# Optimization experiments

Measured on AMD Instinct MI355X. Metric: run time of the kernel, lower is better.

The kernel has to match this reference:

```python
import jax, jax.numpy as jnp
import numpy as np
from jax import lax

B_, L_, C_IN = 32, 1024, 3
D_MODEL, D_STATE, D_CONV, EXPAND = 256, 16, 4, 2
D_INNER = EXPAND * D_MODEL           # 512
DT_RANK = D_MODEL // 16              # 16
N_HEADS, N_CLASS = 8, 10
LN_EPS = 1e-5


def _pos_emb(L, d):
    pos = np.arange(L, dtype=np.float32)[:, None]
    div = np.exp(np.arange(0, d, 2, dtype=np.float32) * (-np.log(10000.0) / d))
    pe = np.zeros((L, d), np.float32)
    pe[:, 0::2] = np.sin(pos * div)
    pe[:, 1::2] = np.cos(pos * div)
    return jnp.asarray(pe)


def setup_inputs() -> dict:
    key = jax.random.key(0)
    ks = jax.random.split(key, 12)
    f = lambda k, shp, s: jax.random.normal(k, shp, jnp.float32) * s
    return {
        'x_enc': f(ks[0], (B_, L_, C_IN), 1.0),
        'x_mark_enc': jnp.ones((B_, L_), jnp.float32),
        'conv_emb_w': f(ks[1], (D_MODEL, C_IN, 3), (2.0 / (C_IN * 3)) ** 0.5),
        'in_proj_w': f(ks[2], (2 * D_INNER, D_MODEL), D_MODEL ** -0.5),
        'conv1d_w': f(ks[3], (D_INNER, 1, D_CONV), D_CONV ** -0.5),
        'conv1d_b': f(ks[4], (D_INNER,), 0.02),
        'x_proj_w': f(ks[5], (DT_RANK + 2 * D_STATE, D_INNER), D_INNER ** -0.5),
        'dt_proj_w': f(ks[6], (D_INNER, DT_RANK), DT_RANK ** -0.5),
        'dt_proj_b': f(ks[7], (D_INNER,), 0.1) - 2.0,
        'A_log': jnp.log(jnp.tile(jnp.arange(1, D_STATE + 1, dtype=jnp.float32), (D_INNER, 1))),
        'D': jnp.ones((D_INNER,), jnp.float32),
        'out_proj_w': f(ks[8], (D_MODEL, D_INNER), D_INNER ** -0.5),
        'ln_g': jnp.ones((D_MODEL,), jnp.float32),
        'ln_b': jnp.zeros((D_MODEL,), jnp.float32),
        'out_w': f(ks[9], (N_CLASS, D_MODEL), D_MODEL ** -0.5),
        'attn_w': f(ks[10], (N_HEADS, D_MODEL), 0.02),
        'attn_b': jnp.ones((N_HEADS,), jnp.float32),
    }


def _forward(x_enc, x_mark_enc, conv_emb_w, in_proj_w, conv1d_w, conv1d_b,
             x_proj_w, dt_proj_w, dt_proj_b, A_log, D, out_proj_w,
             ln_g, ln_b, out_w, attn_w, attn_b):
    silu = jax.nn.silu
    # --- embedding: Conv1d 'same' with replicate padding + sinusoidal PE ---
    xp = jnp.pad(x_enc, ((0, 0), (1, 1), (0, 0)), mode='edge')      # k=3 -> pad (1,1)
    x = lax.conv_general_dilated(xp.transpose(0, 2, 1), conv_emb_w, (1,), 'VALID',
                                 dimension_numbers=('NCH', 'OIH', 'NCH')).transpose(0, 2, 1)
    x = x + _pos_emb(L_, D_MODEL)[None]                              # (B,L,D)

    # --- Mamba_TimeVariant (standard Mamba selective scan) ---
    xz = jnp.einsum('bld,ed->ble', x, in_proj_w)                     # (B,L,2*Din)
    xin, z = xz[..., :D_INNER], xz[..., D_INNER:]
    # depthwise causal conv, kernel D_CONV
    xc = jnp.pad(xin.transpose(0, 2, 1), ((0, 0), (0, 0), (D_CONV - 1, 0)))
    xc = lax.conv_general_dilated(xc, conv1d_w, (1,), 'VALID',
                                  feature_group_count=D_INNER,
                                  dimension_numbers=('NCH', 'OIH', 'NCH'))
    xc = silu(xc.transpose(0, 2, 1) + conv1d_b)                      # (B,L,Din)

    dbl = jnp.einsum('bld,ed->ble', xc, x_proj_w)                    # (B,L,dt_rank+2*N)
    dtr = dbl[..., :DT_RANK]
    Bm = dbl[..., DT_RANK:DT_RANK + D_STATE]                         # (B,L,N)
    Cm = dbl[..., DT_RANK + D_STATE:]                                # (B,L,N)
    dt = jax.nn.softplus(jnp.einsum('blr,dr->bld', dtr, dt_proj_w) + dt_proj_b)
    A = -jnp.exp(A_log)                                              # (Din,N)

    def step(h, inp):
        dt_t, B_t, C_t, x_t = inp                                    # (B,Din),(B,N),(B,N),(B,Din)
        dA = jnp.exp(dt_t[..., None] * A)                            # (B,Din,N)
        h = dA * h + dt_t[..., None] * B_t[:, None, :] * x_t[..., None]
        y = jnp.einsum('bdn,bn->bd', h, C_t)
        return h, y

    h0 = jnp.zeros((B_, D_INNER, D_STATE), xc.dtype)
    inputs = (dt.transpose(1, 0, 2), Bm.transpose(1, 0, 2),
              Cm.transpose(1, 0, 2), xc.transpose(1, 0, 2))
    _, ys = lax.scan(step, h0, inputs)                               # (L,B,Din)
    y = ys.transpose(1, 0, 2) + xc * D                               # skip via D
    y = y * silu(z)
    m = jnp.einsum('bld,ed->ble', y, out_proj_w)                     # (B,L,Dmodel)

    # LayerNorm + SiLU
    mu = m.mean(-1, keepdims=True)
    var = ((m - mu) ** 2).mean(-1, keepdims=True)
    m = (m - mu) * lax.rsqrt(var + LN_EPS) * ln_g + ln_b
    m = silu(m)

    # classification head
    logit = jnp.einsum('bld,cd->blc', m, out_w) * x_mark_enc[..., None]
    s = jnp.einsum('bld,hd->blh', m, attn_w) + attn_b                # (B,L,H)
    w = jax.nn.softmax(jnp.max(s, axis=2, keepdims=True), axis=1)    # (B,L,1)
    return (logit * w).sum(1)                                        # (B,num_class)


def reference(x_enc, x_mark_enc, conv_emb_w, in_proj_w, conv1d_w, conv1d_b,
              x_proj_w, dt_proj_w, dt_proj_b, A_log, D, out_proj_w,
              ln_g, ln_b, out_w, attn_w, attn_b):
    return _forward(x_enc, x_mark_enc, conv_emb_w, in_proj_w, conv1d_w, conv1d_b,
                    x_proj_w, dt_proj_w, dt_proj_b, A_log, D, out_proj_w,
                    ln_g, ln_b, out_w, attn_w, attn_b)
```

## Files before the change

### kernel.cpp

```cpp
#include <hip/hip_runtime.h>
#include <hip/hip_bf16.h>
#include <math.h>

#define B_  32
#define L_  1024
#define CIN 3
#define DM  256
#define DI  512
#define NST 16
#define NH  8
#define NC  10
#define M_TOT (B_*L_)

typedef unsigned short u16;
typedef __attribute__((ext_vector_type(8))) short bf16x8;
typedef __attribute__((ext_vector_type(4))) float f32x4;

static __device__ __forceinline__ float sigmoidf_(float x) {
    return 1.0f / (1.0f + __expf(-x));
}
static __device__ __forceinline__ u16 f2bf(float f) {
    unsigned int u = __float_as_uint(f);
    return (u16)((u + 0x7FFF + ((u >> 16) & 1)) >> 16);
}
static __device__ __forceinline__ float bf2f(u16 u) {
    return __uint_as_float(((unsigned int)u) << 16);
}

static __device__ __forceinline__ void reduce16_pair(float& a, float& b) {
    asm volatile(
        "s_nop 1\n\t"
        "v_add_f32 %0, %0, %0 quad_perm:[1,0,3,2] row_mask:0xf bank_mask:0xf\n\t"
        "v_add_f32 %1, %1, %1 quad_perm:[1,0,3,2] row_mask:0xf bank_mask:0xf\n\t"
        "s_nop 1\n\t"
        "v_add_f32 %0, %0, %0 quad_perm:[2,3,0,1] row_mask:0xf bank_mask:0xf\n\t"
        "v_add_f32 %1, %1, %1 quad_perm:[2,3,0,1] row_mask:0xf bank_mask:0xf\n\t"
        "s_nop 1\n\t"
        "v_add_f32 %0, %0, %0 row_ror:4 row_mask:0xf bank_mask:0xf\n\t"
        "v_add_f32 %1, %1, %1 row_ror:4 row_mask:0xf bank_mask:0xf\n\t"
        "s_nop 1\n\t"
        "v_add_f32 %0, %0, %0 row_ror:8 row_mask:0xf bank_mask:0xf\n\t"
        "v_add_f32 %1, %1, %1 row_ror:8 row_mask:0xf bank_mask:0xf\n\t"
        "s_nop 1\n\t"
        : "+v"(a), "+v"(b));
}

__global__ __launch_bounds__(256) void k_cvt(const float* __restrict__ in,
        u16* __restrict__ out) {
    int i = (blockIdx.x * 256 + threadIdx.x) * 4;
    float4 v = *(const float4*)(in + i);
    ushort4 o;
    o.x = f2bf(v.x); o.y = f2bf(v.y); o.z = f2bf(v.z); o.w = f2bf(v.w);
    *(ushort4*)(out + i) = o;
}

__global__ __launch_bounds__(256) void k_embed(const float* __restrict__ xe,
        const float* __restrict__ w, u16* __restrict__ x) {
    int bl = blockIdx.x;
    int l = bl & (L_-1);
    int b = bl >> 10;
    int d = threadIdx.x;
    const float* xb = xe + (size_t)b * L_ * CIN;
    int t0 = l > 0 ? l-1 : 0;
    int t2 = l < L_-1 ? l+1 : L_-1;
    const float* w3 = w + d*9;
    float acc = 0.f;
    #pragma unroll
    for (int i = 0; i < 3; ++i) {
        acc += xb[t0*3+i] * w3[i*3+0];
        acc += xb[l *3+i] * w3[i*3+1];
        acc += xb[t2*3+i] * w3[i*3+2];
    }
    int j = d >> 1;
    float div = expf((float)(2*j) * (-logf(10000.0f)/(float)DM));
    float ang = (float)l * div;
    acc += (d & 1) ? cosf(ang) : sinf(ang);
    x[(size_t)bl*DM + d] = f2bf(acc);
}

#define GST 40
__global__ __launch_bounds__(256) void k_gemm_mfma(
        const u16* __restrict__ A, const u16* __restrict__ W,
        float* __restrict__ O1f, u16* __restrict__ O1b,
        u16* __restrict__ O2b, int M, int N, int K, int S) {
    __shared__ u16 As[128*GST];
    __shared__ u16 Bs[128*GST];
    int tid = threadIdx.x;
    int row0 = blockIdx.y * 128, col0 = blockIdx.x * 128;
    int wave = tid >> 6, lane = tid & 63;
    int wr = (wave >> 1) * 64, wc = (wave & 1) * 64;
    int l16 = lane & 15, kl = lane >> 4;
    int srow = tid >> 1, skh = (tid & 1) * 16;
    const u16* Ag = A + (size_t)(row0 + srow) * K + skh;
    const u16* Wg = W + (size_t)(col0 + srow) * K + skh;

    f32x4 acc[4][4];
    #pragma unroll
    for (int m = 0; m < 4; ++m)
        #pragma unroll
        for (int n = 0; n < 4; ++n)
            acc[m][n] = (f32x4){0.f, 0.f, 0.f, 0.f};

    for (int k0 = 0; k0 < K; k0 += 32) {
        uint4 a0 = *(const uint4*)(Ag + k0);
        uint4 a1 = *(const uint4*)(Ag + k0 + 8);
        uint4 b0 = *(const uint4*)(Wg + k0);
        uint4 b1 = *(const uint4*)(Wg + k0 + 8);
        __syncthreads();
        *(uint4*)&As[srow*GST + skh]     = a0;
        *(uint4*)&As[srow*GST + skh + 8] = a1;
        *(uint4*)&Bs[srow*GST + skh]     = b0;
        *(uint4*)&Bs[srow*GST + skh + 8] = b1;
        __syncthreads();
        bf16x8 af[4], bf[4];
        #pragma unroll
        for (int m = 0; m < 4; ++m)
            af[m] = *(const bf16x8*)&As[(wr + m*16 + l16)*GST + kl*8];
        #pragma unroll
        for (int n = 0; n < 4; ++n)
            bf[n] = *(const bf16x8*)&Bs[(wc + n*16 + l16)*GST + kl*8];
        #pragma unroll
        for (int m = 0; m < 4; ++m)
            #pragma unroll
            for (int n = 0; n < 4; ++n)
                acc[m][n] = __builtin_amdgcn_mfma_f32_16x16x32_bf16(
                                af[m], bf[n], acc[m][n], 0, 0, 0);
    }

    #pragma unroll
    for (int m = 0; m < 4; ++m) {
        int rbase = row0 + wr + m*16 + kl*4;
        #pragma unroll
        for (int n = 0; n < 4; ++n) {
            int col = col0 + wc + n*16 + l16;
            #pragma unroll
            for (int r = 0; r < 4; ++r) {
                float v = acc[m][n][r];
                if (col < S) {
                    if (O1b) O1b[(size_t)(rbase + r)*S + col] = f2bf(v);
                    else     O1f[(size_t)(rbase + r)*S + col] = v;
                } else {
                    O2b[(size_t)(rbase + r)*(N - S) + (col - S)] = f2bf(v);
                }
            }
        }
    }
}

__global__ __launch_bounds__(256) void k_conv(const u16* __restrict__ xin,
        const float* __restrict__ w, const float* __restrict__ bias,
        u16* __restrict__ xc) {
    size_t i4 = (size_t)blockIdx.x * 256 + threadIdx.x;
    int d4 = (int)(i4 & (DI/4 - 1)) * 4;
    size_t m = i4 >> 7;
    int l = (int)(m & (L_-1));
    float4 wv0 = *(const float4*)(w + (size_t)(d4+0)*4);
    float4 wv1 = *(const float4*)(w + (size_t)(d4+1)*4);
    float4 wv2 = *(const float4*)(w + (size_t)(d4+2)*4);
    float4 wv3 = *(const float4*)(w + (size_t)(d4+3)*4);
    float W[4][4] = {{wv0.x,wv0.y,wv0.z,wv0.w},{wv1.x,wv1.y,wv1.z,wv1.w},
                     {wv2.x,wv2.y,wv2.z,wv2.w},{wv3.x,wv3.y,wv3.z,wv3.w}};
    float4 acc = *(const float4*)(bias + d4);
    #pragma unroll
    for (int k = 0; k < 4; ++k) {
        int t = l + k - 3;
        if (t >= 0) {
            ushort4 xv = *(const ushort4*)(xin + (m + k - 3)*DI + d4);
            acc.x = fmaf(bf2f(xv.x), W[0][k], acc.x);
            acc.y = fmaf(bf2f(xv.y), W[1][k], acc.y);
            acc.z = fmaf(bf2f(xv.z), W[2][k], acc.z);
            acc.w = fmaf(bf2f(xv.w), W[3][k], acc.w);
        }
    }
    ushort4 r;
    r.x = f2bf(acc.x * sigmoidf_(acc.x));
    r.y = f2bf(acc.y * sigmoidf_(acc.y));
    r.z = f2bf(acc.z * sigmoidf_(acc.z));
    r.w = f2bf(acc.w * sigmoidf_(acc.w));
    *(ushort4*)(xc + m*DI + d4) = r;
}

#define XBM 128
#define XBK 16
__global__ __launch_bounds__(256) void k_xproj(const u16* __restrict__ xc,
        const float* __restrict__ wp, float* __restrict__ dbl) {
    __shared__ float As[XBK][XBM];
    __shared__ float Ws[XBK][48];
    int tid = threadIdx.x;
    int row0 = blockIdx.x * XBM;
    int lr = tid >> 1;
    int lk = (tid & 1) * 8;
    int we = tid >> 2;
    int wk = (tid & 3) * 4;
    int tx = tid & 15;
    int ty = tid >> 4;
    float acc[8][3];
    #pragma unroll
    for (int i = 0; i < 8; ++i)
        #pragma unroll
        for (int j = 0; j < 3; ++j) acc[i][j] = 0.f;

    for (int k0 = 0; k0 < DI; k0 += XBK) {
        ushort4 ab0 = *(const ushort4*)(xc + (size_t)(row0+lr)*DI + k0 + lk);
        ushort4 ab1 = *(const ushort4*)(xc + (size_t)(row0+lr)*DI + k0 + lk + 4);
        float4 w0 = make_float4(0.f,0.f,0.f,0.f);
        if (tid < 192) w0 = *(const float4*)(wp + (size_t)we*DI + k0 + wk);
        __syncthreads();
        As[lk+0][lr]=bf2f(ab0.x); As[lk+1][lr]=bf2f(ab0.y);
        As[lk+2][lr]=bf2f(ab0.z); As[lk+3][lr]=bf2f(ab0.w);
        As[lk+4][lr]=bf2f(ab1.x); As[lk+5][lr]=bf2f(ab1.y);
        As[lk+6][lr]=bf2f(ab1.z); As[lk+7][lr]=bf2f(ab1.w);
        if (tid < 192) {
            Ws[wk+0][we]=w0.x; Ws[wk+1][we]=w0.y; Ws[wk+2][we]=w0.z; Ws[wk+3][we]=w0.w;
        }
        __syncthreads();
        #pragma unroll
        for (int k = 0; k < XBK; ++k) {
            float4 av0 = *(const float4*)&As[k][ty*8];
            float4 av1 = *(const float4*)&As[k][ty*8+4];
            float w0_ = Ws[k][tx*3+0];
            float w1_ = Ws[k][tx*3+1];
            float w2_ = Ws[k][tx*3+2];
            float ar[8] = {av0.x,av0.y,av0.z,av0.w,av1.x,av1.y,av1.z,av1.w};
            #pragma unroll
            for (int i = 0; i < 8; ++i) {
                acc[i][0] = fmaf(ar[i], w0_, acc[i][0]);
                acc[i][1] = fmaf(ar[i], w1_, acc[i][1]);
                acc[i][2] = fmaf(ar[i], w2_, acc[i][2]);
            }
        }
    }
    #pragma unroll
    for (int i = 0; i < 8; ++i) {
        size_t r = row0 + ty*8 + i;
        #pragma unroll
        for (int j = 0; j < 3; ++j)
            dbl[r*48 + tx*3 + j] = acc[i][j];
    }
}

__global__ __launch_bounds__(256) void k_dtproj(const float* __restrict__ dbl,
        const float* __restrict__ dtw, const float* __restrict__ dtb,
        float* __restrict__ dt) {
    __shared__ float wl[DI][17];
    __shared__ float rl[32][16];
    size_t m0 = (size_t)blockIdx.x * 32;
    for (int i = threadIdx.x; i < DI*16; i += 256)
        wl[i >> 4][i & 15] = dtw[i];
    for (int i = threadIdx.x; i < 32*16; i += 256)
        rl[i >> 4][i & 15] = dbl[(m0 + (i>>4))*48 + (i & 15)];
    __syncthreads();
    float b0 = dtb[threadIdx.x];
    float b1 = dtb[256 + threadIdx.x];
    for (int mm = 0; mm < 32; ++mm) {
        #pragma unroll
        for (int half = 0; half < 2; ++half) {
            int d = half*256 + threadIdx.x;
            float acc = half ? b1 : b0;
            #pragma unroll
            for (int r = 0; r < 16; ++r)
                acc = fmaf(rl[mm][r], wl[d][r], acc);
            float sp = fmaxf(acc, 0.f) + log1pf(__expf(-fabsf(acc)));
            dt[(m0+mm)*DI + d] = sp;
        }
    }
}

#define SCAN_T 64
__global__ __launch_bounds__(256) void k_scan(const float* __restrict__ dt,
        const u16* __restrict__ xcb, const float* __restrict__ dbl,
        const float* __restrict__ A_log, const float* __restrict__ Dp,
        const u16* __restrict__ zbf, u16* __restrict__ ybf) {
    __shared__ float4 sq4[SCAN_T*17];
    __shared__ float2 sBC2[SCAN_T*17];

    int tid = threadIdx.x;
    int ch = tid >> 4;
    int n  = tid & 15;
    int d0 = blockIdx.x * 16;
    int b  = blockIdx.y;
    int d  = d0 + ch;
    float Avl2 = -expf(A_log[(size_t)d*NST + n]) * 1.44269504f;
    float h = 0.f;
    size_t base = (size_t)b * L_;

    int st = tid >> 2;
    int sc = (tid & 3) * 4;
    float4 Dv = *(const float4*)(Dp + d0 + sc);

    for (int t0 = 0; t0 < L_; t0 += SCAN_T) {
        __syncthreads();
        {
            size_t row = base + t0 + st;
            float4 dtv = *(const float4*)(dt + row*DI + d0 + sc);
            ushort4 xv4 = *(const ushort4*)(xcb + row*DI + d0 + sc);
            ushort4 zv4 = *(const ushort4*)(zbf + row*DI + d0 + sc);
            float4 Bv  = *(const float4*)(dbl + row*48 + 16 + sc);
            float4 Cv  = *(const float4*)(dbl + row*48 + 32 + sc);
            float x0 = bf2f(xv4.x), x1 = bf2f(xv4.y);
            float x2 = bf2f(xv4.z), x3 = bf2f(xv4.w);
            float z0 = bf2f(zv4.x), z1 = bf2f(zv4.y);
            float z2 = bf2f(zv4.z), z3 = bf2f(zv4.w);
            float g0 = z0 * sigmoidf_(z0);
            float g1 = z1 * sigmoidf_(z1);
            float g2 = z2 * sigmoidf_(z2);
            float g3 = z3 * sigmoidf_(z3);
            sq4[st*17 + sc+0] = make_float4(dtv.x, dtv.x*x0, x0*Dv.x*g0, g0);
            sq4[st*17 + sc+1] = make_float4(dtv.y, dtv.y*x1, x1*Dv.y*g1, g1);
            sq4[st*17 + sc+2] = make_float4(dtv.z, dtv.z*x2, x2*Dv.z*g2, g2);
            sq4[st*17 + sc+3] = make_float4(dtv.w, dtv.w*x3, x3*Dv.w*g3, g3);
            sBC2[st*17 + sc+0] = make_float2(Bv.x, Cv.x);
            sBC2[st*17 + sc+1] = make_float2(Bv.y, Cv.y);
            sBC2[st*17 + sc+2] = make_float2(Bv.z, Cv.z);
            sBC2[st*17 + sc+3] = make_float2(Bv.w, Cv.w);
        }
        __syncthreads();

        #pragma unroll 2
        for (int t2 = 0; t2 < SCAN_T/2; ++t2) {
            float2 bc0 = sBC2[(2*t2)*17 + n];
            float2 bc1 = sBC2[(2*t2+1)*17 + n];
            float4 q0 = sq4[(2*t2)*17 + ch];
            float4 q1 = sq4[(2*t2+1)*17 + ch];
            float dA = exp2f(q0.x * Avl2);
            h = fmaf(dA, h, q0.y * bc0.x);
            float p0 = h * bc0.y;
            dA = exp2f(q1.x * Avl2);
            h = fmaf(dA, h, q1.y * bc1.x);
            float p1 = h * bc1.y;
            reduce16_pair(p0, p1);
            if (n == 0) {
                size_t row = base + t0 + 2*t2;
                ybf[row*DI + d]     = f2bf(fmaf(p0, q0.w, q0.z));
                ybf[(row+1)*DI + d] = f2bf(fmaf(p1, q1.w, q1.z));
            }
        }
    }
}

__global__ __launch_bounds__(256) void k_lnsilu(float* __restrict__ m,
        const float* __restrict__ g, const float* __restrict__ bta) {
    size_t row = (size_t)blockIdx.x*4 + (threadIdx.x >> 6);
    int lane = threadIdx.x & 63;
    float4 v = *(const float4*)(m + row*DM + lane*4);
    float s = v.x + v.y + v.z + v.w;
    #pragma unroll
    for (int o = 32; o > 0; o >>= 1) s += __shfl_xor(s, o);
    float mu = s * (1.0f/DM);
    float4 c = make_float4(v.x-mu, v.y-mu, v.z-mu, v.w-mu);
    float s2 = c.x*c.x + c.y*c.y + c.z*c.z + c.w*c.w;
    #pragma unroll
    for (int o = 32; o > 0; o >>= 1) s2 += __shfl_xor(s2, o);
    float rstd = 1.0f / sqrtf(s2 * (1.0f/DM) + 1e-5f);
    float4 gv = *(const float4*)(g + lane*4);
    float4 bv = *(const float4*)(bta + lane*4);
    float o0 = c.x*rstd*gv.x + bv.x;
    float o1 = c.y*rstd*gv.y + bv.y;
    float o2 = c.z*rstd*gv.z + bv.z;
    float o3 = c.w*rstd*gv.w + bv.w;
    float4 r;
    r.x = o0 * sigmoidf_(o0);
    r.y = o1 * sigmoidf_(o1);
    r.z = o2 * sigmoidf_(o2);
    r.w = o3 * sigmoidf_(o3);
    *(float4*)(m + row*DM + lane*4) = r;
}

#define HBK 32
__global__ __launch_bounds__(256) void k_heads18(const float* __restrict__ m,
        const float* __restrict__ aw, const float* __restrict__ ow,
        float* __restrict__ r18) {
    __shared__ float As[128][36];
    __shared__ float Ws[18][36];
    int tid = threadIdx.x;
    int row0 = blockIdx.x * 128;
    int r = tid >> 1, ch = tid & 1, cb = ch * 9;
    int sr = tid >> 1, sk = (tid & 1) * 16;
    float acc[9];
    #pragma unroll
    for (int c = 0; c < 9; ++c) acc[c] = 0.f;

    for (int k0 = 0; k0 < DM; k0 += HBK) {
        float4 a[4];
        #pragma unroll
        for (int q = 0; q < 4; ++q)
            a[q] = *(const float4*)(m + (size_t)(row0+sr)*DM + k0 + sk + q*4);
        float4 wv = make_float4(0.f,0.f,0.f,0.f);
        int wc = tid >> 3, wk = (tid & 7) * 4;
        if (tid < 144) {
            const float* wsrc = (wc < NH) ? (aw + wc*DM) : (ow + (wc-NH)*DM);
            wv = *(const float4*)(wsrc + k0 + wk);
        }
        __syncthreads();
        #pragma unroll
        for (int q = 0; q < 4; ++q)
            *(float4*)&As[sr][sk + q*4] = a[q];
        if (tid < 144)
            *(float4*)&Ws[wc][wk] = wv;
        __syncthreads();
        #pragma unroll
        for (int k4 = 0; k4 < HBK/4; ++k4) {
            float4 av = *(const float4*)&As[r][k4*4];
            #pragma unroll
            for (int c = 0; c < 9; ++c) {
                float4 w4 = *(const float4*)&Ws[cb + c][k4*4];
                acc[c] += av.x*w4.x + av.y*w4.y + av.z*w4.z + av.w*w4.w;
            }
        }
        __syncthreads();
    }
    #pragma unroll
    for (int c = 0; c < 9; ++c)
        r18[(size_t)(row0 + r)*18 + cb + c] = acc[c];
}

__global__ __launch_bounds__(256) void k_final(const float* __restrict__ r18,
        const float* __restrict__ ab, const float* __restrict__ xmark,
        float* __restrict__ out) {
    __shared__ float e[L_];
    __shared__ float red[256];
    int b = blockIdx.x;
    int tid = threadIdx.x;
    float abr[NH];
    #pragma unroll
    for (int j = 0; j < NH; ++j) abr[j] = ab[j];
    float mx = -1e30f;
    for (int l = tid; l < L_; l += 256) {
        const float* rr = r18 + ((size_t)b*L_ + l)*18;
        float sm = rr[0] + abr[0];
        #pragma unroll
        for (int j = 1; j < NH; ++j) sm = fmaxf(sm, rr[j] + abr[j]);
        e[l] = sm;
        mx = fmaxf(mx, sm);
    }
    #pragma unroll
    for (int o = 32; o > 0; o >>= 1) mx = fmaxf(mx, __shfl_xor(mx, o));
    red[tid] = mx;
    __syncthreads();
    mx = fmaxf(fmaxf(red[0], red[64]), fmaxf(red[128], red[192]));
    __syncthreads();
    float ssum = 0.f;
    for (int l = tid; l < L_; l += 256) {
        float ev = __expf(e[l] - mx);
        e[l] = ev;
        ssum += ev;
    }
    #pragma unroll
    for (int o = 32; o > 0; o >>= 1) ssum += __shfl_xor(ssum, o);
    if ((tid & 63) == 0) red[tid >> 6] = ssum;
    __syncthreads();
    float inv = 1.0f / (red[0]+red[1]+red[2]+red[3]);
    float acc[NC];
    #pragma unroll
    for (int c = 0; c < NC; ++c) acc[c] = 0.f;
    for (int l = tid; l < L_; l += 256) {
        float wl = e[l] * xmark[(size_t)b*L_ + l];
        const float* lg = r18 + ((size_t)b*L_ + l)*18 + NH;
        #pragma unroll
        for (int c = 0; c < NC; ++c) acc[c] = fmaf(wl, lg[c], acc[c]);
    }
    __syncthreads();
    for (int c = 0; c < NC; ++c) {
        red[tid] = acc[c];
        __syncthreads();
        if (tid < 64) {
            float s2 = red[tid]+red[tid+64]+red[tid+128]+red[tid+192];
            #pragma unroll
            for (int o = 32; o > 0; o >>= 1) s2 += __shfl_xor(s2, o);
            if (tid == 0) out[(size_t)b*NC + c] = s2 * inv;
        }
        __syncthreads();
    }
}

extern "C" void kernel_launch(void* const* d_in, const int* in_sizes, int n_in,
                              void* d_out, int out_size, void* d_ws, size_t ws_size,
                              hipStream_t stream) {
    const float* x_enc  = (const float*)d_in[0];
    const float* x_mark = (const float*)d_in[1];
    const float* cemb_w = (const float*)d_in[2];
    const float* inp_w  = (const float*)d_in[3];
    const float* c1_w   = (const float*)d_in[4];
    const float* c1_b   = (const float*)d_in[5];
    const float* xp_w   = (const float*)d_in[6];
    const float* dtp_w  = (const float*)d_in[7];
    const float* dtp_b  = (const float*)d_in[8];
    const float* A_log  = (const float*)d_in[9];
    const float* Dp     = (const float*)d_in[10];
    const float* outp_w = (const float*)d_in[11];
    const float* ln_g   = (const float*)d_in[12];
    const float* ln_b   = (const float*)d_in[13];
    const float* out_w  = (const float*)d_in[14];
    const float* attn_w = (const float*)d_in[15];
    const float* attn_b = (const float*)d_in[16];
    float* out = (float*)d_out;

    char* ws = (char*)d_ws;
    size_t o = 0;
    u16*   xbf  = (u16*)(ws + o);   o += (size_t)M_TOT*DM*2;
    u16*   xinb = (u16*)(ws + o);   o += (size_t)M_TOT*DI*2;
    u16*   zbf  = (u16*)(ws + o);   o += (size_t)M_TOT*DI*2;
    u16*   xcb  = (u16*)(ws + o);   o += (size_t)M_TOT*DI*2;
    u16*   ybf  = (u16*)(ws + o);   o += (size_t)M_TOT*DI*2;
    float* dt   = (float*)(ws + o); o += (size_t)M_TOT*DI*4;
    float* mm   = (float*)(ws + o); o += (size_t)M_TOT*DM*4;
    float* dbl  = (float*)(ws + o); o += (size_t)M_TOT*48*4;
    u16*   wbfi = (u16*)(ws + o);   o += (size_t)2*DI*DM*2;
    u16*   wbfo = (u16*)(ws + o);   o += (size_t)DM*DI*2;
    float* r18  = (float*)(ws + o); o += (size_t)M_TOT*18*4;

    k_cvt   <<<(2*DI*DM)/1024, 256, 0, stream>>>(inp_w, wbfi);
    k_cvt   <<<(DM*DI)/1024, 256, 0, stream>>>(outp_w, wbfo);
    k_embed <<<M_TOT, 256, 0, stream>>>(x_enc, cemb_w, xbf);
    k_gemm_mfma<<<dim3(8, M_TOT/128), 256, 0, stream>>>(xbf, wbfi,
                                nullptr, xinb, zbf, M_TOT, 2*DI, DM, DI);
    k_conv  <<<(M_TOT*DI/4)/256, 256, 0, stream>>>(xinb, c1_w, c1_b, xcb);
    k_xproj <<<M_TOT/XBM, 256, 0, stream>>>(xcb, xp_w, dbl);
    k_dtproj<<<M_TOT/32, 256, 0, stream>>>(dbl, dtp_w, dtp_b, dt);
    k_scan  <<<dim3(DI/16, B_), 256, 0, stream>>>(dt, xcb, dbl, A_log, Dp,
                                                  zbf, ybf);
    k_gemm_mfma<<<dim3(2, M_TOT/128), 256, 0, stream>>>(ybf, wbfo,
                                mm, nullptr, zbf, M_TOT, DM, DI, DM);
    k_lnsilu<<<M_TOT/4, 256, 0, stream>>>(mm, ln_g, ln_b);
    k_heads18<<<M_TOT/128, 256, 0, stream>>>(mm, attn_w, out_w, r18);
    k_final <<<B_, 256, 0, stream>>>(r18, attn_b, x_mark, out);
}
```

Before: 465.1 us.

## Give each scan thread two SSM states and 32 channels per block

Result: no change. 463.3 us (-0.4%).

```diff
diff --git a/kernel.cpp b/kernel.cpp
--- a/kernel.cpp
+++ b/kernel.cpp
@@ -27,7 +27,7 @@
     return __uint_as_float(((unsigned int)u) << 16);
 }
 
-static __device__ __forceinline__ void reduce16_pair(float& a, float& b) {
+static __device__ __forceinline__ void reduce8_pair(float& a, float& b) {
     asm volatile(
         "s_nop 1\n\t"
         "v_add_f32 %0, %0, %0 quad_perm:[1,0,3,2] row_mask:0xf bank_mask:0xf\n\t"
@@ -36,11 +36,8 @@
         "v_add_f32 %0, %0, %0 quad_perm:[2,3,0,1] row_mask:0xf bank_mask:0xf\n\t"
         "v_add_f32 %1, %1, %1 quad_perm:[2,3,0,1] row_mask:0xf bank_mask:0xf\n\t"
         "s_nop 1\n\t"
-        "v_add_f32 %0, %0, %0 row_ror:4 row_mask:0xf bank_mask:0xf\n\t"
-        "v_add_f32 %1, %1, %1 row_ror:4 row_mask:0xf bank_mask:0xf\n\t"
-        "s_nop 1\n\t"
-        "v_add_f32 %0, %0, %0 row_ror:8 row_mask:0xf bank_mask:0xf\n\t"
-        "v_add_f32 %1, %1, %1 row_ror:8 row_mask:0xf bank_mask:0xf\n\t"
+        "v_add_f32 %0, %0, %0 row_half_mirror row_mask:0xf bank_mask:0xf\n\t"
+        "v_add_f32 %1, %1, %1 row_half_mirror row_mask:0xf bank_mask:0xf\n\t"
         "s_nop 1\n\t"
         : "+v"(a), "+v"(b));
 }
@@ -271,65 +268,79 @@
         const u16* __restrict__ xcb, const float* __restrict__ dbl,
         const float* __restrict__ A_log, const float* __restrict__ Dp,
         const u16* __restrict__ zbf, u16* __restrict__ ybf) {
-    __shared__ float4 sq4[SCAN_T*17];
-    __shared__ float2 sBC2[SCAN_T*17];
+    __shared__ float4 sq4[SCAN_T*33];
+    __shared__ float2 sBC2[SCAN_T*18];
 
     int tid = threadIdx.x;
-    int ch = tid >> 4;
-    int n  = tid & 15;
-    int d0 = blockIdx.x * 16;
+    int wave = tid >> 6, lane = tid & 63;
+    int chw = lane >> 3;
+    int j   = lane & 7;
+    int ch  = wave*8 + chw;
+    int d0 = blockIdx.x * 32;
     int b  = blockIdx.y;
     int d  = d0 + ch;
-    float Avl2 = -expf(A_log[(size_t)d*NST + n]) * 1.44269504f;
-    float h = 0.f;
+    float Aa = -expf(A_log[(size_t)d*NST + 2*j])     * 1.44269504f;
+    float Ab = -expf(A_log[(size_t)d*NST + 2*j + 1]) * 1.44269504f;
+    float h0 = 0.f, h1 = 0.f;
     size_t base = (size_t)b * L_;
 
     int st = tid >> 2;
-    int sc = (tid & 3) * 4;
-    float4 Dv = *(const float4*)(Dp + d0 + sc);
+    int sc = (tid & 3) * 8;
+    int ns = (tid & 3) * 4;
+    float4 Dva = *(const float4*)(Dp + d0 + sc);
+    float4 Dvb = *(const float4*)(Dp + d0 + sc + 4);
 
     for (int t0 = 0; t0 < L_; t0 += SCAN_T) {
         __syncthreads();
         {
             size_t row = base + t0 + st;
-            float4 dtv = *(const float4*)(dt + row*DI + d0 + sc);
-            ushort4 xv4 = *(const ushort4*)(xcb + row*DI + d0 + sc);
-            ushort4 zv4 = *(const ushort4*)(zbf + row*DI + d0 + sc);
-            float4 Bv  = *(const float4*)(dbl + row*48 + 16 + sc);
-            float4 Cv  = *(const float4*)(dbl + row*48 + 32 + sc);
-            float x0 = bf2f(xv4.x), x1 = bf2f(xv4.y);
-            float x2 = bf2f(xv4.z), x3 = bf2f(xv4.w);
-            float z0 = bf2f(zv4.x), z1 = bf2f(zv4.y);
-            float z2 = bf2f(zv4.z), z3 = bf2f(zv4.w);
-            float g0 = z0 * sigmoidf_(z0);
-            float g1 = z1 * sigmoidf_(z1);
-            float g2 = z2 * sigmoidf_(z2);
-            float g3 = z3 * sigmoidf_(z3);
-            sq4[st*17 + sc+0] = make_float4(dtv.x, dtv.x*x0, x0*Dv.x*g0, g0);
-            sq4[st*17 + sc+1] = make_float4(dtv.y, dtv.y*x1, x1*Dv.y*g1, g1);
-            sq4[st*17 + sc+2] = make_float4(dtv.z, dtv.z*x2, x2*Dv.z*g2, g2);
-            sq4[st*17 + sc+3] = make_float4(dtv.w, dtv.w*x3, x3*Dv.w*g3, g3);
-            sBC2[st*17 + sc+0] = make_float2(Bv.x, Cv.x);
-            sBC2[st*17 + sc+1] = make_float2(Bv.y, Cv.y);
-            sBC2[st*17 + sc+2] = make_float2(Bv.z, Cv.z);
-            sBC2[st*17 + sc+3] = make_float2(Bv.w, Cv.w);
+            float4 dtv0 = *(const float4*)(dt + row*DI + d0 + sc);
+            float4 dtv1 = *(const float4*)(dt + row*DI + d0 + sc + 4);
+            uint4 xv = *(const uint4*)(xcb + row*DI + d0 + sc);
+            uint4 zv = *(const uint4*)(zbf + row*DI + d0 + sc);
+            float4 Bv = *(const float4*)(dbl + row*48 + 16 + ns);
+            float4 Cv = *(const float4*)(dbl + row*48 + 32 + ns);
+            float xr[8] = { bf2f((u16)(xv.x & 0xffff)), bf2f((u16)(xv.x >> 16)),
+                            bf2f((u16)(xv.y & 0xffff)), bf2f((u16)(xv.y >> 16)),
+                            bf2f((u16)(xv.z & 0xffff)), bf2f((u16)(xv.z >> 16)),
+                            bf2f((u16)(xv.w & 0xffff)), bf2f((u16)(xv.w >> 16)) };
+            float zr[8] = { bf2f((u16)(zv.x & 0xffff)), bf2f((u16)(zv.x >> 16)),
+                            bf2f((u16)(zv.y & 0xffff)), bf2f((u16)(zv.y >> 16)),
+                            bf2f((u16)(zv.z & 0xffff)), bf2f((u16)(zv.z >> 16)),
+                            bf2f((u16)(zv.w & 0xffff)), bf2f((u16)(zv.w >> 16)) };
+            float dtr[8] = { dtv0.x, dtv0.y, dtv0.z, dtv0.w,
+                             dtv1.x, dtv1.y, dtv1.z, dtv1.w };
+            float Dr[8] = { Dva.x, Dva.y, Dva.z, Dva.w,
+                            Dvb.x, Dvb.y, Dvb.z, Dvb.w };
+            #pragma unroll
+            for (int k = 0; k < 8; ++k) {
+                float g = zr[k] * sigmoidf_(zr[k]);
+                sq4[st*33 + sc + k] = make_float4(dtr[k], dtr[k]*xr[k],
+                                                  xr[k]*Dr[k]*g, g);
+            }
+            *(float4*)&sBC2[st*18 + ns]     = make_float4(Bv.x, Cv.x, Bv.y, Cv.y);
+            *(float4*)&sBC2[st*18 + ns + 2] = make_float4(Bv.z, Cv.z, Bv.w, Cv.w);
         }
         __syncthreads();
 
         #pragma unroll 2
         for (int t2 = 0; t2 < SCAN_T/2; ++t2) {
-            float2 bc0 = sBC2[(2*t2)*17 + n];
-            float2 bc1 = sBC2[(2*t2+1)*17 + n];
-            float4 q0 = sq4[(2*t2)*17 + ch];
-            float4 q1 = sq4[(2*t2+1)*17 + ch];
-            float dA = exp2f(q0.x * Avl2);
-            h = fmaf(dA, h, q0.y * bc0.x);
-            float p0 = h * bc0.y;
-            dA = exp2f(q1.x * Avl2);
-            h = fmaf(dA, h, q1.y * bc1.x);
-            float p1 = h * bc1.y;
-            reduce16_pair(p0, p1);
-            if (n == 0) {
+            float4 bc0 = *(const float4*)&sBC2[(2*t2)*18 + 2*j];
+            float4 bc1 = *(const float4*)&sBC2[(2*t2+1)*18 + 2*j];
+            float4 q0 = sq4[(2*t2)*33 + ch];
+            float4 q1 = sq4[(2*t2+1)*33 + ch];
+            float dA0 = exp2f(q0.x * Aa);
+            float dA1 = exp2f(q0.x * Ab);
+            h0 = fmaf(dA0, h0, q0.y * bc0.x);
+            h1 = fmaf(dA1, h1, q0.y * bc0.z);
+            float p0 = fmaf(h1, bc0.w, h0 * bc0.y);
+            dA0 = exp2f(q1.x * Aa);
+            dA1 = exp2f(q1.x * Ab);
+            h0 = fmaf(dA0, h0, q1.y * bc1.x);
+            h1 = fmaf(dA1, h1, q1.y * bc1.z);
+            float p1 = fmaf(h1, bc1.w, h0 * bc1.y);
+            reduce8_pair(p0, p1);
+            if (j == 0) {
                 size_t row = base + t0 + 2*t2;
                 ybf[row*DI + d]     = f2bf(fmaf(p0, q0.w, q0.z));
                 ybf[(row+1)*DI + d] = f2bf(fmaf(p1, q1.w, q1.z));
@@ -517,7 +528,7 @@
     k_conv  <<<(M_TOT*DI/4)/256, 256, 0, stream>>>(xinb, c1_w, c1_b, xcb);
     k_xproj <<<M_TOT/XBM, 256, 0, stream>>>(xcb, xp_w, dbl);
     k_dtproj<<<M_TOT/32, 256, 0, stream>>>(dbl, dtp_w, dtp_b, dt);
-    k_scan  <<<dim3(DI/16, B_), 256, 0, stream>>>(dt, xcb, dbl, A_log, Dp,
+    k_scan  <<<dim3(DI/32, B_), 256, 0, stream>>>(dt, xcb, dbl, A_log, Dp,
                                                   zbf, ybf);
     k_gemm_mfma<<<dim3(2, M_TOT/128), 256, 0, stream>>>(ybf, wbfo,
                                 mm, nullptr, zbf, M_TOT, DM, DI, DM);
```
